# Kernel tuning notes

Hardware: AMD Instinct MI355X
Metric: run time of the kernel (lower is better)

Reference implementation:

```python
import jax, jax.numpy as jnp
import numpy as np

B, S, H, M, STEPS = 8, 1024, 1024, 4, 5
LN_EPS = 1e-5


def _gelu(x):
    return jax.nn.gelu(x, approximate=False)  # torch nn.GELU default is exact erf


def _layernorm(x, g, b):
    mu = jnp.mean(x, axis=-1, keepdims=True)
    var = jnp.mean((x - mu) ** 2, axis=-1, keepdims=True)
    return (x - mu) * jax.lax.rsqrt(var + LN_EPS) * g + b


def setup_inputs() -> dict:
    key = jax.random.key(0)
    ks = jax.random.split(key, 16)
    def w(k, shape, scale=0.02):
        return (jax.random.normal(k, shape) * scale).astype(jnp.float32)
    z = lambda *shape: jnp.zeros(shape, jnp.float32)
    o = lambda *shape: jnp.ones(shape, jnp.float32)
    return {
        "deterministic_state": jax.random.normal(ks[0], (B, S, H), jnp.float32),
        "superposition_state": jax.random.normal(ks[1], (B, S, H * M), jnp.float32),
        "context": jax.random.normal(ks[2], (B, H), jnp.float32),
        # reasoning_mode_selector: Linear(H,H) -> GELU -> Linear(H,2) -> Softmax
        "Wm1": w(ks[3], (H, H)), "bm1": z(H), "Wm2": w(ks[4], (H, 2)), "bm2": z(2),
        # reasoning_depth_controller: Linear(H,H//2) -> GELU -> Linear(H//2,STEPS) -> Softmax
        "Wd1": w(ks[5], (H, H // 2)), "bd1": z(H // 2), "Wd2": w(ks[6], (H // 2, STEPS)), "bd2": z(STEPS),
        # explicit_reasoning_steps (stacked over STEPS): Linear(2H,H)->GELU->Linear(H,H)->LayerNorm
        "We1": w(ks[7], (STEPS, 2 * H, H)), "be1": z(STEPS, H),
        "We2": w(ks[8], (STEPS, H, H)), "be2": z(STEPS, H),
        "ln_g": o(STEPS, H), "ln_b": z(STEPS, H),
        # reasoning_memory GRUCell(H,H); gate order r,z,n as in torch
        "W_ih": w(ks[9], (H, 3 * H)), "W_hh": w(ks[10], (H, 3 * H)),
        "b_ih": z(3 * H), "b_hh": z(3 * H),
        # implicit_reasoning: Linear(H*M,2H)->GELU->Linear(2H,H*M)->LayerNorm
        "Wi1": w(ks[11], (H * M, 2 * H)), "bi1": z(2 * H),
        "Wi2": w(ks[12], (2 * H, H * M)), "bi2": z(H * M),
        "lni_g": o(H * M), "lni_b": z(H * M),
    }


def _forward(deterministic_state, superposition_state, context,
             Wm1, bm1, Wm2, bm2, Wd1, bd1, Wd2, bd2,
             We1, be1, We2, be2, ln_g, ln_b,
             W_ih, W_hh, b_ih, b_hh,
             Wi1, bi1, Wi2, bi2, lni_g, lni_b):
    b, s, h = deterministic_state.shape
    # mode / depth selection from 2D context [B,H]
    mode_weights = jax.nn.softmax(_gelu(context @ Wm1 + bm1) @ Wm2 + bm2, axis=-1)   # [B,2]
    depth_weights = jax.nn.softmax(_gelu(context @ Wd1 + bd1) @ Wd2 + bd2, axis=-1)  # [B,STEPS]

    ctx_exp = jnp.broadcast_to(context[:, None, :], (b, s, h))  # context.unsqueeze(1).expand

    def gru_cell(x, hprev):  # x,hprev: [N,H]
        gi = x @ W_ih + b_ih
        gh = hprev @ W_hh + b_hh
        i_r, i_z, i_n = jnp.split(gi, 3, axis=-1)
        h_r, h_z, h_n = jnp.split(gh, 3, axis=-1)
        r = jax.nn.sigmoid(i_r + h_r)
        z = jax.nn.sigmoid(i_z + h_z)
        n = jnp.tanh(i_n + r * h_n)
        return (1.0 - z) * n + z * hprev

    def step(carry, params):
        state, memory = carry
        W1, b1, W2, b2, g, beta = params
        combined = jnp.concatenate([state, ctx_exp], axis=-1)          # [B,S,2H]
        next_state = _layernorm(_gelu(combined @ W1 + b1) @ W2 + b2, g, beta)
        mem = gru_cell(next_state.reshape(-1, h), memory.reshape(-1, h)).reshape(b, s, h)
        gated = next_state + 0.1 * mem
        return (gated, mem), gated

    init = (deterministic_state, jnp.zeros_like(deterministic_state))
    _, gated_states = jax.lax.scan(step, init, (We1, be1, We2, be2, ln_g, ln_b))  # [STEPS,B,S,H]
    explicit_result = jnp.einsum('bi,ibsh->bsh', depth_weights, gated_states)

    implicit_result = _layernorm(_gelu(superposition_state @ Wi1 + bi1) @ Wi2 + bi2, lni_g, lni_b)  # [B,S,M*H]
    implicit_det = implicit_result.reshape(b, s, M, h).mean(axis=2)  # [B,S,H]

    result = (mode_weights[:, 0, None, None] * implicit_det
              + mode_weights[:, 1, None, None] * explicit_result)
    return result, mode_weights, depth_weights, explicit_result, implicit_result


def reference(deterministic_state, superposition_state, context,
              Wm1, bm1, Wm2, bm2, Wd1, bd1, Wd2, bd2,
              We1, be1, We2, be2, ln_g, ln_b,
              W_ih, W_hh, b_ih, b_hh,
              Wi1, bi1, Wi2, bi2, lni_g, lni_b):
    return _forward(deterministic_state, superposition_state, context,
                    Wm1, bm1, Wm2, bm2, Wd1, bd1, Wd2, bd2,
                    We1, be1, We2, be2, ln_g, ln_b,
                    W_ih, W_hh, b_ih, b_hh,
                    Wi1, bi1, Wi2, bi2, lni_g, lni_b)
```

## Files before the change

### kernel.cpp

```cpp
#include <hip/hip_runtime.h>
#include <hip/hip_bf16.h>
#include <math.h>


typedef unsigned short bf16_t;
typedef __attribute__((ext_vector_type(8))) short s8v;
typedef __attribute__((ext_vector_type(4))) float f4v;

typedef const __attribute__((address_space(1))) void* gas_ptr;
typedef __attribute__((address_space(3))) void* las_ptr;

#define DEVFN static __device__ __forceinline__

DEVFN bf16_t f2b(float f) {
    union { float f; unsigned u; } v; v.f = f;
    unsigned r = v.u + 0x7FFFu + ((v.u >> 16) & 1u);
    return (bf16_t)(r >> 16);
}
DEVFN float b2f(bf16_t b) {
    union { unsigned u; float f; } v; v.u = ((unsigned)b) << 16; return v.f;
}
DEVFN float geluf(float x) { return 0.5f * x * (1.0f + erff(x * 0.70710678118654752f)); }
DEVFN float sigmf(float x) { return 1.0f / (1.0f + expf(-x)); }

template <int N_> DEVFN void waitvm() {
    if constexpr (N_ == 7)  asm volatile("s_waitcnt vmcnt(7)"  ::: "memory");
    if constexpr (N_ == 9)  asm volatile("s_waitcnt vmcnt(9)"  ::: "memory");
    if constexpr (N_ == 10) asm volatile("s_waitcnt vmcnt(10)" ::: "memory");
    if constexpr (N_ == 12) asm volatile("s_waitcnt vmcnt(12)" ::: "memory");
    __builtin_amdgcn_sched_barrier(0);
}
DEVFN void lgkm0() {
    asm volatile("s_waitcnt lgkmcnt(0)" ::: "memory");
    __builtin_amdgcn_sched_barrier(0);
}

static const long OUT_RESULT = 0;
static const long OUT_MODE   = 8388608;
static const long OUT_DEPTH  = 8388624;
static const long OUT_EXPL   = 8388664;
static const long OUT_IMPL   = 16777272;

#define READ_AH(mh, c_) { _Pragma("unroll") \
    for (int mf = 0; mf < MF / 2; ++mf) { _Pragma("unroll") \
      for (int ks = 0; ks < 2; ++ks) { \
        aR[mf][ks] = *(const s8v*)(lds + (c_) * BUFB + \
            ((mh) * (BM / 2) + wm * (BM / 4) + mf * 16 + l15) * 128 + \
            ((((ks << 2) + lhi) ^ l7) << 4)); } } }

#define READ_BH(nh, c_, dst) { _Pragma("unroll") \
    for (int nf = 0; nf < NF / 2; ++nf) { _Pragma("unroll") \
      for (int ks = 0; ks < 2; ++ks) { \
        dst[nf][ks] = *(const s8v*)(lds + (c_) * BUFB + ABYTES + \
            ((nh) * (BN / 2) + wn * (BN / 8) + nf * 16 + l15) * 128 + \
            ((((ks << 2) + lhi) ^ l7) << 4)); } } }

#define MFMA_Q(mh, nh, bset) { __builtin_amdgcn_s_setprio(1); _Pragma("unroll") \
    for (int mf = 0; mf < MF / 2; ++mf) { _Pragma("unroll") \
      for (int nf = 0; nf < NF / 2; ++nf) { _Pragma("unroll") \
        for (int ks = 0; ks < 2; ++ks) { \
          acc[(mh) * (MF / 2) + mf][(nh) * (NF / 2) + nf] = \
            __builtin_amdgcn_mfma_f32_16x16x32_bf16(aR[mf][ks], bset[nf][ks], \
                acc[(mh) * (MF / 2) + mf][(nh) * (NF / 2) + nf], 0, 0, 0); } } } \
    __builtin_amdgcn_s_setprio(0); }

template <int MF, int NF, int EPI>
__global__ __launch_bounds__(512, 2) void gemm8p(
    const bf16_t* __restrict__ A, const bf16_t* __restrict__ Bt,
    const float* __restrict__ bias, bf16_t* __restrict__ outB, int N, int K)
{
    constexpr int BM = MF * 32;
    constexpr int BN = NF * 64;
    constexpr int LA = BM / 64;
    constexpr int LB = BN / 64;
    constexpr int sA = LA / 2;
    constexpr int sB = LB / 2;
    constexpr int V1 = 3 * sA + 2 * sB;
    constexpr int V24 = 3 * (sA + sB);
    constexpr int ABYTES = BM * 128;
    constexpr int BUFB = (BM + BN) * 128;

    __shared__ __align__(16) char lds[2 * BUFB];

    const int tid  = threadIdx.x;
    const int lane = tid & 63;
    const int wave = tid >> 6;
    const int wm = wave >> 2, wn = wave & 3;
    const int l15 = lane & 15, lhi = lane >> 4, l7 = lane & 7;

    const int gx = gridDim.x;
    const int nwg = gx * gridDim.y;
    const int orig = blockIdx.y * gx + blockIdx.x;
    const int qq = nwg >> 3, rr8 = nwg & 7;
    const int xcd = orig & 7, lid = orig >> 3;
    const int nid = (xcd < rr8 ? xcd * (qq + 1) : rr8 * (qq + 1) + (xcd - rr8) * qq) + lid;
    const int m0 = (nid / gx) * BM;
    const int n0 = (nid % gx) * BN;

    const int NT = K >> 6;

    f4v acc[MF][NF];
#pragma unroll
    for (int i = 0; i < MF; ++i)
#pragma unroll
        for (int j = 0; j < NF; ++j)
#pragma unroll
            for (int q2 = 0; q2 < 4; ++q2) acc[i][j][q2] = 0.0f;

    s8v aR[MF / 2][2];
    s8v bR0[NF / 2][2], bR1[NF / 2][2];

    auto stageA = [&](int ts, int tb, int h) {
        const int kt = ts << 6;
#pragma unroll
        for (int i = 0; i < sA; ++i) {
            const int li = (h * sA + i) * 512 + tid;
            const int r = li >> 3, s = li & 7;
            const bf16_t* src = A + (long)(m0 + r) * K + kt + ((s ^ (r & 7)) << 3);
            __builtin_amdgcn_global_load_lds((gas_ptr)src, (las_ptr)(lds + tb * BUFB + li * 16), 16, 0, 0);
        }
    };
    auto stageB = [&](int ts, int tb, int h) {
        const int kt = ts << 6;
#pragma unroll
        for (int i = 0; i < sB; ++i) {
            const int li = (h * sB + i) * 512 + tid;
            const int r = li >> 3, s = li & 7;
            const bf16_t* src = Bt + (long)(n0 + r) * K + kt + ((s ^ (r & 7)) << 3);
            __builtin_amdgcn_global_load_lds((gas_ptr)src, (las_ptr)(lds + tb * BUFB + ABYTES + li * 16), 16, 0, 0);
        }
    };

    stageA(0, 0, 0); stageB(0, 0, 0); stageB(0, 0, 1); stageA(0, 0, 1);
    stageA(1, 1, 0); stageB(1, 1, 0); stageB(1, 1, 1); stageA(1, 1, 1);
    waitvm<V24>();
    __builtin_amdgcn_s_barrier();

    for (int t = 0; t < NT; ++t) {
        const int c = t & 1;
        int ts = t + 2; if (ts >= NT) ts -= NT;
        READ_AH(0, c);
        READ_BH(0, c, bR0);
        waitvm<V1>();
        __builtin_amdgcn_s_barrier();
        lgkm0();
        MFMA_Q(0, 0, bR0);
        __builtin_amdgcn_s_barrier();
        READ_BH(1, c, bR1);
        stageA(ts, c, 0); stageB(ts, c, 0);
        waitvm<V24>();
        __builtin_amdgcn_s_barrier();
        lgkm0();
        MFMA_Q(0, 1, bR1);
        __builtin_amdgcn_s_barrier();
        READ_AH(1, c);
        stageB(ts, c, 1);
        __builtin_amdgcn_s_barrier();
        lgkm0();
        MFMA_Q(1, 1, bR1);
        __builtin_amdgcn_s_barrier();
        stageA(ts, c, 1);
        waitvm<V24>();
        __builtin_amdgcn_s_barrier();
        MFMA_Q(1, 0, bR0);
        __builtin_amdgcn_s_barrier();
    }

    const int crr = lhi << 2;
#pragma unroll
    for (int mh = 0; mh < 2; ++mh) {
#pragma unroll
        for (int mf = 0; mf < MF / 2; ++mf) {
#pragma unroll
            for (int nh = 0; nh < 2; ++nh) {
#pragma unroll
                for (int nf = 0; nf < NF / 2; ++nf) {
                    const int col = n0 + nh * (BN / 2) + wn * (BN / 8) + nf * 16 + l15;
#pragma unroll
                    for (int q2 = 0; q2 < 4; ++q2) {
                        const int row = m0 + mh * (BM / 2) + wm * (BM / 4) + mf * 16 + crr + q2;
                        const float v = acc[mh * (MF / 2) + mf][nh * (NF / 2) + nf][q2];
                        if (EPI == 1) {
                            outB[(long)row * N + col] = f2b(geluf(v + bias[col]));
                        } else if (EPI == 2) {
                            outB[(long)row * N + col] = f2b(geluf(v + bias[(long)(row >> 10) * N + col]));
                        } else {
                            outB[(long)row * N + col] = f2b(v + bias[col]);
                        }
                    }
                }
            }
        }
    }
}

__global__ __launch_bounds__(256) void transpose_k(
    const float* __restrict__ src, bf16_t* __restrict__ dst,
    int K, int N, long sbs, long dbs)
{
    __shared__ float tile[32][33];
    const float* s = src + (long)blockIdx.z * sbs;
    bf16_t* d = dst + (long)blockIdx.z * dbs;
    const int n0 = blockIdx.x * 32, k0 = blockIdx.y * 32;
    const int tx = threadIdx.x, ty = threadIdx.y;
#pragma unroll
    for (int i = 0; i < 4; ++i)
        tile[ty + i * 8][tx] = s[(long)(k0 + ty + i * 8) * N + n0 + tx];
    __syncthreads();
#pragma unroll
    for (int i = 0; i < 4; ++i)
        d[(long)(n0 + ty + i * 8) * K + k0 + tx] = f2b(tile[tx][ty + i * 8]);
}

__global__ __launch_bounds__(256) void cvt_k(const float4* __restrict__ src,
                                             ushort4* __restrict__ dst, int n4)
{
    const int i = blockIdx.x * 256 + threadIdx.x;
    if (i < n4) {
        float4 v = src[i];
        ushort4 o; o.x = f2b(v.x); o.y = f2b(v.y); o.z = f2b(v.z); o.w = f2b(v.w);
        dst[i] = o;
    }
}

__global__ __launch_bounds__(256) void colgemv8_k(
    const float* __restrict__ ctx, const float* __restrict__ Wbase, long wts,
    int Wld, const float* __restrict__ bias, long bts,
    float* __restrict__ out, long ots, int do_gelu)
{
    __shared__ float cs[8][1024];
    __shared__ float rr[16][16][8];
    const int j0 = blockIdx.x * 16;
    const int t = blockIdx.y;
    const int tid = threadIdx.x;
    for (int i = tid; i < 2048; i += 256)
        ((float4*)cs)[i] = ((const float4*)ctx)[i];
    __syncthreads();
    const int kp = tid >> 4, jj = tid & 15;
    const float* Wp = Wbase + (long)t * wts;
    float p[8] = {0, 0, 0, 0, 0, 0, 0, 0};
    for (int i = 0; i < 64; ++i) {
        const int k = kp * 64 + i;
        const float w = Wp[(long)k * Wld + j0 + jj];
#pragma unroll
        for (int b = 0; b < 8; ++b) p[b] = fmaf(cs[b][k], w, p[b]);
    }
#pragma unroll
    for (int b = 0; b < 8; ++b) rr[kp][jj][b] = p[b];
    __syncthreads();
    if (tid < 128) {
        const int jj2 = tid >> 3, b = tid & 7;
        float s = 0.f;
#pragma unroll
        for (int k2 = 0; k2 < 16; ++k2) s += rr[k2][jj2][b];
        s += bias[(long)t * bts + j0 + jj2];
        if (do_gelu) s = geluf(s);
        out[(long)t * ots + (long)b * Wld + j0 + jj2] = s;
    }
}

__global__ __launch_bounds__(256) void selB_k(
    const float* __restrict__ h1, const float* __restrict__ hd,
    const float* __restrict__ Wm2, const float* __restrict__ bm2,
    const float* __restrict__ Wd2, const float* __restrict__ bd2,
    float* __restrict__ outM, float* __restrict__ outD,
    float* __restrict__ wsM, float* __restrict__ wsD)
{
    const int b = blockIdx.x, tid = threadIdx.x;
    __shared__ float red[256];
    float lm[2], ld[5];
    for (int o = 0; o < 2; ++o) {
        float p = 0.f;
        for (int k = tid; k < 1024; k += 256) p += h1[b * 1024 + k] * Wm2[k * 2 + o];
        red[tid] = p; __syncthreads();
        for (int s = 128; s > 0; s >>= 1) { if (tid < s) red[tid] += red[tid + s]; __syncthreads(); }
        lm[o] = red[0] + bm2[o]; __syncthreads();
    }
    for (int o = 0; o < 5; ++o) {
        float p = 0.f;
        for (int k = tid; k < 512; k += 256) p += hd[b * 512 + k] * Wd2[k * 5 + o];
        red[tid] = p; __syncthreads();
        for (int s = 128; s > 0; s >>= 1) { if (tid < s) red[tid] += red[tid + s]; __syncthreads(); }
        ld[o] = red[0] + bd2[o]; __syncthreads();
    }
    if (tid == 0) {
        float mx = fmaxf(lm[0], lm[1]);
        float e0 = expf(lm[0] - mx), e1 = expf(lm[1] - mx);
        float inv = 1.f / (e0 + e1);
        outM[b * 2] = e0 * inv; outM[b * 2 + 1] = e1 * inv;
        wsM[b * 2] = e0 * inv;  wsM[b * 2 + 1] = e1 * inv;
        float md = ld[0];
        for (int o = 1; o < 5; ++o) md = fmaxf(md, ld[o]);
        float es[5]; float sum = 0.f;
        for (int o = 0; o < 5; ++o) { es[o] = expf(ld[o] - md); sum += es[o]; }
        for (int o = 0; o < 5; ++o) { outD[b * 5 + o] = es[o] / sum; wsD[b * 5 + o] = es[o] / sum; }
    }
}

__global__ __launch_bounds__(256) void ln1024_k(
    const bf16_t* __restrict__ X, const float* __restrict__ g,
    const float* __restrict__ b, bf16_t* __restrict__ Yb)
{
    const int row = blockIdx.x, tid = threadIdx.x;
    const ushort4 xv = ((const ushort4*)(X + (long)row * 1024))[tid];
    const float x0 = b2f(xv.x), x1 = b2f(xv.y), x2 = b2f(xv.z), x3 = b2f(xv.w);
    float s = x0 + x1 + x2 + x3;
    float ss = x0 * x0 + x1 * x1 + x2 * x2 + x3 * x3;
#pragma unroll
    for (int o = 32; o > 0; o >>= 1) { s += __shfl_down(s, o); ss += __shfl_down(ss, o); }
    __shared__ float rs[4], rss[4];
    const int wv = tid >> 6, ln = tid & 63;
    if (ln == 0) { rs[wv] = s; rss[wv] = ss; }
    __syncthreads();
    const float S = rs[0] + rs[1] + rs[2] + rs[3];
    const float SS = rss[0] + rss[1] + rss[2] + rss[3];
    const float mean = S * (1.0f / 1024.0f);
    const float var = SS * (1.0f / 1024.0f) - mean * mean;
    const float rstd = rsqrtf(var + 1e-5f);
    const float4 gv = ((const float4*)g)[tid];
    const float4 bv = ((const float4*)b)[tid];
    ushort4 ob;
    ob.x = f2b((x0 - mean) * rstd * gv.x + bv.x);
    ob.y = f2b((x1 - mean) * rstd * gv.y + bv.y);
    ob.z = f2b((x2 - mean) * rstd * gv.z + bv.z);
    ob.w = f2b((x3 - mean) * rstd * gv.w + bv.w);
    ((ushort4*)(Yb + (long)row * 1024))[tid] = ob;
}

template <bool FIRST>
__global__ __launch_bounds__(256) void gru_k(
    const bf16_t* __restrict__ gi, const bf16_t* __restrict__ gh,
    const float* __restrict__ bhh, const bf16_t* __restrict__ nsB,
    bf16_t* __restrict__ memB, bf16_t* __restrict__ stateB,
    float* __restrict__ expl, const float* __restrict__ depthw, int t)
{
    const long i4 = (long)blockIdx.x * 256 + threadIdx.x;
    const long row = i4 >> 8;
    const int h4 = (int)(i4 & 255) << 2;
    const bf16_t* gir = gi + row * 3072 + h4;
    const ushort4 vir = *(const ushort4*)(gir);
    const ushort4 viz = *(const ushort4*)(gir + 1024);
    const ushort4 vin = *(const ushort4*)(gir + 2048);
    float hr[4], hz[4], hn[4];
    if (FIRST) {
        const float4 a = *(const float4*)(bhh + h4);
        const float4 c = *(const float4*)(bhh + 1024 + h4);
        const float4 d = *(const float4*)(bhh + 2048 + h4);
        hr[0] = a.x; hr[1] = a.y; hr[2] = a.z; hr[3] = a.w;
        hz[0] = c.x; hz[1] = c.y; hz[2] = c.z; hz[3] = c.w;
        hn[0] = d.x; hn[1] = d.y; hn[2] = d.z; hn[3] = d.w;
    } else {
        const bf16_t* ghr = gh + row * 3072 + h4;
        const ushort4 g1 = *(const ushort4*)(ghr);
        const ushort4 g2 = *(const ushort4*)(ghr + 1024);
        const ushort4 g3 = *(const ushort4*)(ghr + 2048);
        hr[0] = b2f(g1.x); hr[1] = b2f(g1.y); hr[2] = b2f(g1.z); hr[3] = b2f(g1.w);
        hz[0] = b2f(g2.x); hz[1] = b2f(g2.y); hz[2] = b2f(g2.z); hz[3] = b2f(g2.w);
        hn[0] = b2f(g3.x); hn[1] = b2f(g3.y); hn[2] = b2f(g3.z); hn[3] = b2f(g3.w);
    }
    const ushort4 nsv = *(const ushort4*)(nsB + row * 1024 + h4);
    float mo[4] = {0.f, 0.f, 0.f, 0.f};
    if (!FIRST) {
        const ushort4 mv = *(const ushort4*)(memB + row * 1024 + h4);
        mo[0] = b2f(mv.x); mo[1] = b2f(mv.y); mo[2] = b2f(mv.z); mo[3] = b2f(mv.w);
    }
    const float dw = depthw[(int)(row >> 10) * 5 + t];
    const float ir[4] = {b2f(vir.x), b2f(vir.y), b2f(vir.z), b2f(vir.w)};
    const float iz[4] = {b2f(viz.x), b2f(viz.y), b2f(viz.z), b2f(viz.w)};
    const float in_[4] = {b2f(vin.x), b2f(vin.y), b2f(vin.z), b2f(vin.w)};
    const float ns[4] = {b2f(nsv.x), b2f(nsv.y), b2f(nsv.z), b2f(nsv.w)};
    ushort4 mnb, stb; float4 exv;
    float mn[4], gt[4];
#pragma unroll
    for (int i = 0; i < 4; ++i) {
        const float rg = sigmf(ir[i] + hr[i]);
        const float zg = sigmf(iz[i] + hz[i]);
        const float ng = tanhf(in_[i] + rg * hn[i]);
        mn[i] = (1.0f - zg) * ng + zg * mo[i];
        gt[i] = ns[i] + 0.1f * mn[i];
    }
    mnb.x = f2b(mn[0]); mnb.y = f2b(mn[1]); mnb.z = f2b(mn[2]); mnb.w = f2b(mn[3]);
    stb.x = f2b(gt[0]); stb.y = f2b(gt[1]); stb.z = f2b(gt[2]); stb.w = f2b(gt[3]);
    exv.x = dw * gt[0]; exv.y = dw * gt[1]; exv.z = dw * gt[2]; exv.w = dw * gt[3];
    *(ushort4*)(memB + row * 1024 + h4) = mnb;
    *(ushort4*)(stateB + row * 1024 + h4) = stb;
    float* ep = expl + row * 1024 + h4;
    if (FIRST) {
        *(float4*)ep = exv;
    } else {
        float4 old = *(const float4*)ep;
        old.x += exv.x; old.y += exv.y; old.z += exv.z; old.w += exv.w;
        *(float4*)ep = old;
    }
}

__global__ __launch_bounds__(1024) void ln4096_final_k(
    const bf16_t* __restrict__ Ypre, const float* __restrict__ g,
    const float* __restrict__ b, const float* __restrict__ expl,
    float* __restrict__ implOut, float* __restrict__ result,
    const float* __restrict__ modew)
{
    const int row = blockIdx.x, tid = threadIdx.x;
    const ushort4 xv = ((const ushort4*)(Ypre + (long)row * 4096))[tid];
    const float x0 = b2f(xv.x), x1 = b2f(xv.y), x2 = b2f(xv.z), x3 = b2f(xv.w);
    float s = x0 + x1 + x2 + x3;
    float ss = x0 * x0 + x1 * x1 + x2 * x2 + x3 * x3;
#pragma unroll
    for (int o = 32; o > 0; o >>= 1) { s += __shfl_down(s, o); ss += __shfl_down(ss, o); }
    __shared__ float rs[16], rss[16];
    __shared__ float ylds[4096];
    const int wv = tid >> 6, ln = tid & 63;
    if (ln == 0) { rs[wv] = s; rss[wv] = ss; }
    __syncthreads();
    if (tid < 64) {
        float a = (ln < 16) ? rs[ln] : 0.f;
        float c2 = (ln < 16) ? rss[ln] : 0.f;
#pragma unroll
        for (int o = 8; o > 0; o >>= 1) { a += __shfl_down(a, o); c2 += __shfl_down(c2, o); }
        if (ln == 0) { rs[0] = a; rss[0] = c2; }
    }
    __syncthreads();
    const float mean = rs[0] * (1.f / 4096.f);
    const float var = rss[0] * (1.f / 4096.f) - mean * mean;
    const float rstd = rsqrtf(var + 1e-5f);
    const float4 gv = ((const float4*)g)[tid];
    const float4 bv = ((const float4*)b)[tid];
    float4 y;
    y.x = (x0 - mean) * rstd * gv.x + bv.x;
    y.y = (x1 - mean) * rstd * gv.y + bv.y;
    y.z = (x2 - mean) * rstd * gv.z + bv.z;
    y.w = (x3 - mean) * rstd * gv.w + bv.w;
    ((float4*)(implOut + (long)row * 4096))[tid] = y;
    ((float4*)ylds)[tid] = y;
    __syncthreads();
    const int bidx = row >> 10;
    const float det4 = 0.25f * (ylds[tid] + ylds[tid + 1024] + ylds[tid + 2048] + ylds[tid + 3072]);
    result[(long)row * 1024 + tid] = modew[bidx * 2] * det4
                                   + modew[bidx * 2 + 1] * expl[(long)row * 1024 + tid];
}

extern "C" void kernel_launch(void* const* d_in, const int* in_sizes, int n_in,
                              void* d_out, int out_size, void* d_ws, size_t ws_size,
                              hipStream_t stream)
{
    const float* det    = (const float*)d_in[0];
    const float* super_ = (const float*)d_in[1];
    const float* ctx    = (const float*)d_in[2];
    const float* Wm1 = (const float*)d_in[3];
    const float* bm1 = (const float*)d_in[4];
    const float* Wm2 = (const float*)d_in[5];
    const float* bm2 = (const float*)d_in[6];
    const float* Wd1 = (const float*)d_in[7];
    const float* bd1 = (const float*)d_in[8];
    const float* Wd2 = (const float*)d_in[9];
    const float* bd2 = (const float*)d_in[10];
    const float* We1 = (const float*)d_in[11];
    const float* be1 = (const float*)d_in[12];
    const float* We2 = (const float*)d_in[13];
    const float* be2 = (const float*)d_in[14];
    const float* ln_g = (const float*)d_in[15];
    const float* ln_b = (const float*)d_in[16];
    const float* W_ih = (const float*)d_in[17];
    const float* W_hh = (const float*)d_in[18];
    const float* b_ih = (const float*)d_in[19];
    const float* b_hh = (const float*)d_in[20];
    const float* Wi1 = (const float*)d_in[21];
    const float* bi1 = (const float*)d_in[22];
    const float* Wi2 = (const float*)d_in[23];
    const float* bi2 = (const float*)d_in[24];
    const float* lni_g = (const float*)d_in[25];
    const float* lni_b = (const float*)d_in[26];

    float* out = (float*)d_out;
    char* W = (char*)d_ws;

    bf16_t* We1sT = (bf16_t*)(W + 0);
    bf16_t* We2T  = (bf16_t*)(W + 10485760L);
    bf16_t* WihT  = (bf16_t*)(W + 20971520L);
    bf16_t* WhhT  = (bf16_t*)(W + 27262976L);
    bf16_t* Wi1T  = (bf16_t*)(W + 33554432L);
    bf16_t* Wi2T  = (bf16_t*)(W + 50331648L);
    float* ctxbias = (float*)(W + 67108864L);
    float* modew   = (float*)(W + 67272704L);
    float* depthw  = (float*)(W + 67272768L);
    float* h1ws    = (float*)(W + 67276800L);
    float* hdws    = (float*)(W + 67309568L);
    const long SB = 67325952L;
    bf16_t* stateb = (bf16_t*)(W + SB);
    bf16_t* Zb     = (bf16_t*)(W + SB + 16777216L);
    bf16_t* memb   = (bf16_t*)(W + SB + 50331648L);
    bf16_t* nsB    = (bf16_t*)(W + SB + 67108864L);
    bf16_t* gi     = (bf16_t*)(W + SB + 83886080L);
    bf16_t* gh     = (bf16_t*)(W + SB + 134217728L);
    bf16_t* Y1     = gi;
    bf16_t* superb = gi;
    bf16_t* Yi     = (bf16_t*)(W + SB + 83886080L + 67108864L);
    bf16_t* Ypre   = gi;

    (void)in_sizes; (void)n_in; (void)out_size; (void)ws_size;

    dim3 tb(32, 8);

    colgemv8_k<<<dim3(64, 1), 256, 0, stream>>>(ctx, Wm1, 0, 1024, bm1, 0, h1ws, 0, 1);
    colgemv8_k<<<dim3(32, 1), 256, 0, stream>>>(ctx, Wd1, 0, 512, bd1, 0, hdws, 0, 1);
    colgemv8_k<<<dim3(64, 5), 256, 0, stream>>>(ctx, We1 + 1048576L, 2097152L, 1024,
                                                be1, 1024, ctxbias, 8192, 0);
    selB_k<<<8, 256, 0, stream>>>(h1ws, hdws, Wm2, bm2, Wd2, bd2,
                                  out + OUT_MODE, out + OUT_DEPTH, modew, depthw);

    transpose_k<<<dim3(32, 32, 5), tb, 0, stream>>>(We1, We1sT, 1024, 1024, 2097152L, 1048576L);
    transpose_k<<<dim3(32, 32, 5), tb, 0, stream>>>(We2, We2T, 1024, 1024, 1048576L, 1048576L);
    transpose_k<<<dim3(96, 32, 1), tb, 0, stream>>>(W_ih, WihT, 1024, 3072, 0L, 0L);
    transpose_k<<<dim3(96, 32, 1), tb, 0, stream>>>(W_hh, WhhT, 1024, 3072, 0L, 0L);
    transpose_k<<<dim3(64, 128, 1), tb, 0, stream>>>(Wi1, Wi1T, 4096, 2048, 0L, 0L);
    transpose_k<<<dim3(128, 64, 1), tb, 0, stream>>>(Wi2, Wi2T, 2048, 4096, 0L, 0L);

    cvt_k<<<8192, 256, 0, stream>>>((const float4*)det, (ushort4*)stateb, 2097152);

    for (int t = 0; t < 5; ++t) {
        gemm8p<4, 4, 2><<<dim3(4, 64), 512, 0, stream>>>(stateb, We1sT + (long)t * 1048576,
                                                         ctxbias + (long)t * 8192, Y1, 1024, 1024);
        gemm8p<4, 4, 3><<<dim3(4, 64), 512, 0, stream>>>(Y1, We2T + (long)t * 1048576,
                                                         be2 + t * 1024, Zb, 1024, 1024);
        ln1024_k<<<8192, 256, 0, stream>>>(Zb, ln_g + t * 1024, ln_b + t * 1024, nsB);
        gemm8p<4, 4, 3><<<dim3(12, 64), 512, 0, stream>>>(nsB, WihT, b_ih, gi, 3072, 1024);
        if (t > 0)
            gemm8p<4, 4, 3><<<dim3(12, 64), 512, 0, stream>>>(memb, WhhT, b_hh, gh, 3072, 1024);
        if (t == 0)
            gru_k<true><<<8192, 256, 0, stream>>>(gi, gh, b_hh, nsB, memb, stateb,
                                                  out + OUT_EXPL, depthw, t);
        else
            gru_k<false><<<8192, 256, 0, stream>>>(gi, gh, b_hh, nsB, memb, stateb,
                                                   out + OUT_EXPL, depthw, t);
    }

    cvt_k<<<32768, 256, 0, stream>>>((const float4*)super_, (ushort4*)superb, 8388608);
    gemm8p<8, 4, 1><<<dim3(8, 32), 512, 0, stream>>>(superb, Wi1T, bi1, Yi, 2048, 4096);
    gemm8p<8, 4, 3><<<dim3(16, 32), 512, 0, stream>>>(Yi, Wi2T, bi2, Ypre, 4096, 2048);
    ln4096_final_k<<<8192, 1024, 0, stream>>>(Ypre, lni_g, lni_b, out + OUT_EXPL,
                                              out + OUT_IMPL, out + OUT_RESULT, modew);
}
```

Measured before the change: 1.482 ms.

## Precompute GEMM address pointers, unroll K loop by two, defer explicit accumulation to final kernel

The GEMM main loop now keeps per-thread global source pointers that are advanced each K tile. LDS read offsets, including the swizzle, are hoisted out of the loop. The loop is unrolled by two with a peeled tail that issues no wasted wraparound loads. The GRU kernel no longer does the fp32 read-modify-write of the explicit result each step; instead every step's bf16 state is kept in a slab and the final layernorm kernel computes the depth-weighted sum. This removes five fp32 read/write passes over the output but adds five bf16 reads and a larger workspace.

After: 1.477 ms. No clear change (-0.3%).

```diff
diff --git a/kernel.cpp b/kernel.cpp
--- a/kernel.cpp
+++ b/kernel.cpp
@@ -41,19 +41,17 @@
 static const long OUT_EXPL   = 8388664;
 static const long OUT_IMPL   = 16777272;
 
-#define READ_AH(mh, c_) { _Pragma("unroll") \
-    for (int mf = 0; mf < MF / 2; ++mf) { _Pragma("unroll") \
-      for (int ks = 0; ks < 2; ++ks) { \
-        aR[mf][ks] = *(const s8v*)(lds + (c_) * BUFB + \
-            ((mh) * (BM / 2) + wm * (BM / 4) + mf * 16 + l15) * 128 + \
-            ((((ks << 2) + lhi) ^ l7) << 4)); } } }
-
-#define READ_BH(nh, c_, dst) { _Pragma("unroll") \
-    for (int nf = 0; nf < NF / 2; ++nf) { _Pragma("unroll") \
-      for (int ks = 0; ks < 2; ++ks) { \
-        dst[nf][ks] = *(const s8v*)(lds + (c_) * BUFB + ABYTES + \
-            ((nh) * (BN / 2) + wn * (BN / 8) + nf * 16 + l15) * 128 + \
-            ((((ks << 2) + lhi) ^ l7) << 4)); } } }
+static const long SLAB = 8388608;
+
+#define RD_A(mh, c_) { _Pragma("unroll") \
+    for (int mf = 0; mf < MF / 2; ++mf) { \
+        aR[mf][0] = *(const s8v*)(lds + (c_) * BUFB + aL + kof0 + ((mh) * (BM / 2) + mf * 16) * 128); \
+        aR[mf][1] = *(const s8v*)(lds + (c_) * BUFB + aL + kof1 + ((mh) * (BM / 2) + mf * 16) * 128); } }
+
+#define RD_B(nh, c_, dst) { _Pragma("unroll") \
+    for (int nf = 0; nf < NF / 2; ++nf) { \
+        dst[nf][0] = *(const s8v*)(lds + (c_) * BUFB + bL + kof0 + ((nh) * (BN / 2) + nf * 16) * 128); \
+        dst[nf][1] = *(const s8v*)(lds + (c_) * BUFB + bL + kof1 + ((nh) * (BN / 2) + nf * 16) * 128); } }
 
 #define MFMA_Q(mh, nh, bset) { __builtin_amdgcn_s_setprio(1); _Pragma("unroll") \
     for (int mf = 0; mf < MF / 2; ++mf) { _Pragma("unroll") \
@@ -63,6 +61,33 @@
             __builtin_amdgcn_mfma_f32_16x16x32_bf16(aR[mf][ks], bset[nf][ks], \
                 acc[(mh) * (MF / 2) + mf][(nh) * (NF / 2) + nf], 0, 0, 0); } } } \
     __builtin_amdgcn_s_setprio(0); }
+
+#define KTILE(c_, STG) {                                            \
+    RD_A(0, c_); RD_B(0, c_, bR0);                                  \
+    waitvm<V1>();                                                   \
+    __builtin_amdgcn_s_barrier();                                   \
+    lgkm0();                                                        \
+    MFMA_Q(0, 0, bR0);                                              \
+    __builtin_amdgcn_s_barrier();                                   \
+    RD_B(1, c_, bR1);                                               \
+    if (STG) { stgA(0, c_); stgB(0, c_); }                          \
+    waitvm<V24>();                                                  \
+    __builtin_amdgcn_s_barrier();                                   \
+    lgkm0();                                                        \
+    MFMA_Q(0, 1, bR1);                                              \
+    __builtin_amdgcn_s_barrier();                                   \
+    RD_A(1, c_);                                                    \
+    if (STG) { stgB(1, c_); }                                       \
+    __builtin_amdgcn_s_barrier();                                   \
+    lgkm0();                                                        \
+    MFMA_Q(1, 1, bR1);                                              \
+    __builtin_amdgcn_s_barrier();                                   \
+    if (STG) { stgA(1, c_); }                                       \
+    waitvm<V24>();                                                  \
+    __builtin_amdgcn_s_barrier();                                   \
+    MFMA_Q(1, 0, bR0);                                              \
+    __builtin_amdgcn_s_barrier();                                   \
+}
 
 template <int MF, int NF, int EPI>
 __global__ __launch_bounds__(512, 2) void gemm8p(
@@ -99,6 +124,13 @@
 
     const int NT = K >> 6;
 
+    const int b2k = l7 >> 2;
+    const int lx  = lhi ^ (l7 & 3);
+    const unsigned aL   = (unsigned)((wm * (BM / 4) + l15) * 128 + (lx << 4));
+    const unsigned bL   = (unsigned)(ABYTES + (wn * (BN / 8) + l15) * 128 + (lx << 4));
+    const unsigned kof0 = (unsigned)(b2k << 6);
+    const unsigned kof1 = (unsigned)((b2k ^ 1) << 6);
+
     f4v acc[MF][NF];
 #pragma unroll
     for (int i = 0; i < MF; ++i)
@@ -110,61 +142,54 @@
     s8v aR[MF / 2][2];
     s8v bR0[NF / 2][2], bR1[NF / 2][2];
 
-    auto stageA = [&](int ts, int tb, int h) {
-        const int kt = ts << 6;
-#pragma unroll
-        for (int i = 0; i < sA; ++i) {
-            const int li = (h * sA + i) * 512 + tid;
-            const int r = li >> 3, s = li & 7;
-            const bf16_t* src = A + (long)(m0 + r) * K + kt + ((s ^ (r & 7)) << 3);
-            __builtin_amdgcn_global_load_lds((gas_ptr)src, (las_ptr)(lds + tb * BUFB + li * 16), 16, 0, 0);
-        }
+    const bf16_t* pA[LA];
+    const bf16_t* pB[LB];
+#pragma unroll
+    for (int i = 0; i < LA; ++i) {
+        const int li = i * 512 + tid;
+        const int r = li >> 3, s = li & 7;
+        pA[i] = A + (long)(m0 + r) * K + ((s ^ (r & 7)) << 3);
+    }
+#pragma unroll
+    for (int i = 0; i < LB; ++i) {
+        const int li = i * 512 + tid;
+        const int r = li >> 3, s = li & 7;
+        pB[i] = Bt + (long)(n0 + r) * K + ((s ^ (r & 7)) << 3);
+    }
+
+    auto stgA = [&](int h, int cbuf) {
+#pragma unroll
+        for (int i = 0; i < sA; ++i)
+            __builtin_amdgcn_global_load_lds((gas_ptr)pA[h * sA + i],
+                (las_ptr)(lds + cbuf * BUFB + (h * sA + i) * 8192 + tid * 16), 16, 0, 0);
     };
-    auto stageB = [&](int ts, int tb, int h) {
-        const int kt = ts << 6;
-#pragma unroll
-        for (int i = 0; i < sB; ++i) {
-            const int li = (h * sB + i) * 512 + tid;
-            const int r = li >> 3, s = li & 7;
-            const bf16_t* src = Bt + (long)(n0 + r) * K + kt + ((s ^ (r & 7)) << 3);
-            __builtin_amdgcn_global_load_lds((gas_ptr)src, (las_ptr)(lds + tb * BUFB + ABYTES + li * 16), 16, 0, 0);
-        }
+    auto stgB = [&](int h, int cbuf) {
+#pragma unroll
+        for (int i = 0; i < sB; ++i)
+            __builtin_amdgcn_global_load_lds((gas_ptr)pB[h * sB + i],
+                (las_ptr)(lds + cbuf * BUFB + ABYTES + (h * sB + i) * 8192 + tid * 16), 16, 0, 0);
     };
-
-    stageA(0, 0, 0); stageB(0, 0, 0); stageB(0, 0, 1); stageA(0, 0, 1);
-    stageA(1, 1, 0); stageB(1, 1, 0); stageB(1, 1, 1); stageA(1, 1, 1);
+    auto adv = [&]() {
+#pragma unroll
+        for (int i = 0; i < LA; ++i) pA[i] += 64;
+#pragma unroll
+        for (int i = 0; i < LB; ++i) pB[i] += 64;
+    };
+
+    stgA(0, 0); stgB(0, 0); stgB(1, 0); stgA(1, 0); adv();
+    stgA(0, 1); stgB(0, 1); stgB(1, 1); stgA(1, 1); adv();
     waitvm<V24>();
     __builtin_amdgcn_s_barrier();
 
-    for (int t = 0; t < NT; ++t) {
-        const int c = t & 1;
-        int ts = t + 2; if (ts >= NT) ts -= NT;
-        READ_AH(0, c);
-        READ_BH(0, c, bR0);
-        waitvm<V1>();
-        __builtin_amdgcn_s_barrier();
-        lgkm0();
-        MFMA_Q(0, 0, bR0);
-        __builtin_amdgcn_s_barrier();
-        READ_BH(1, c, bR1);
-        stageA(ts, c, 0); stageB(ts, c, 0);
-        waitvm<V24>();
-        __builtin_amdgcn_s_barrier();
-        lgkm0();
-        MFMA_Q(0, 1, bR1);
-        __builtin_amdgcn_s_barrier();
-        READ_AH(1, c);
-        stageB(ts, c, 1);
-        __builtin_amdgcn_s_barrier();
-        lgkm0();
-        MFMA_Q(1, 1, bR1);
-        __builtin_amdgcn_s_barrier();
-        stageA(ts, c, 1);
-        waitvm<V24>();
-        __builtin_amdgcn_s_barrier();
-        MFMA_Q(1, 0, bR0);
-        __builtin_amdgcn_s_barrier();
-    }
+    for (int t = 0; t < NT - 2; t += 2) {
+        KTILE(0, true);  adv();
+        KTILE(1, true);  adv();
+    }
+    asm volatile("s_waitcnt vmcnt(0)" ::: "memory");
+    __builtin_amdgcn_sched_barrier(0);
+    __builtin_amdgcn_s_barrier();
+    KTILE(0, false);
+    KTILE(1, false);
 
     const int crr = lhi << 2;
 #pragma unroll
@@ -331,8 +356,7 @@
 __global__ __launch_bounds__(256) void gru_k(
     const bf16_t* __restrict__ gi, const bf16_t* __restrict__ gh,
     const float* __restrict__ bhh, const bf16_t* __restrict__ nsB,
-    bf16_t* __restrict__ memB, bf16_t* __restrict__ stateB,
-    float* __restrict__ expl, const float* __restrict__ depthw, int t)
+    bf16_t* __restrict__ memB, bf16_t* __restrict__ stateOut)
 {
     const long i4 = (long)blockIdx.x * 256 + threadIdx.x;
     const long row = i4 >> 8;
@@ -364,12 +388,11 @@
         const ushort4 mv = *(const ushort4*)(memB + row * 1024 + h4);
         mo[0] = b2f(mv.x); mo[1] = b2f(mv.y); mo[2] = b2f(mv.z); mo[3] = b2f(mv.w);
     }
-    const float dw = depthw[(int)(row >> 10) * 5 + t];
     const float ir[4] = {b2f(vir.x), b2f(vir.y), b2f(vir.z), b2f(vir.w)};
     const float iz[4] = {b2f(viz.x), b2f(viz.y), b2f(viz.z), b2f(viz.w)};
     const float in_[4] = {b2f(vin.x), b2f(vin.y), b2f(vin.z), b2f(vin.w)};
     const float ns[4] = {b2f(nsv.x), b2f(nsv.y), b2f(nsv.z), b2f(nsv.w)};
-    ushort4 mnb, stb; float4 exv;
+    ushort4 mnb, stb;
     float mn[4], gt[4];
 #pragma unroll
     for (int i = 0; i < 4; ++i) {
@@ -381,23 +404,15 @@
     }
     mnb.x = f2b(mn[0]); mnb.y = f2b(mn[1]); mnb.z = f2b(mn[2]); mnb.w = f2b(mn[3]);
     stb.x = f2b(gt[0]); stb.y = f2b(gt[1]); stb.z = f2b(gt[2]); stb.w = f2b(gt[3]);
-    exv.x = dw * gt[0]; exv.y = dw * gt[1]; exv.z = dw * gt[2]; exv.w = dw * gt[3];
     *(ushort4*)(memB + row * 1024 + h4) = mnb;
-    *(ushort4*)(stateB + row * 1024 + h4) = stb;
-    float* ep = expl + row * 1024 + h4;
-    if (FIRST) {
-        *(float4*)ep = exv;
-    } else {
-        float4 old = *(const float4*)ep;
-        old.x += exv.x; old.y += exv.y; old.z += exv.z; old.w += exv.w;
-        *(float4*)ep = old;
-    }
+    *(ushort4*)(stateOut + row * 1024 + h4) = stb;
 }
 
 __global__ __launch_bounds__(1024) void ln4096_final_k(
     const bf16_t* __restrict__ Ypre, const float* __restrict__ g,
-    const float* __restrict__ b, const float* __restrict__ expl,
-    float* __restrict__ implOut, float* __restrict__ result,
+    const float* __restrict__ b, const bf16_t* __restrict__ stS,
+    const float* __restrict__ depthw, float* __restrict__ implOut,
+    float* __restrict__ explOut, float* __restrict__ result,
     const float* __restrict__ modew)
 {
     const int row = blockIdx.x, tid = threadIdx.x;
@@ -434,9 +449,14 @@
     ((float4*)ylds)[tid] = y;
     __syncthreads();
     const int bidx = row >> 10;
+    const long off = (long)row * 1024 + tid;
+    float ex = 0.f;
+#pragma unroll
+    for (int tt = 0; tt < 5; ++tt)
+        ex += depthw[bidx * 5 + tt] * b2f(stS[(long)tt * SLAB + off]);
+    explOut[off] = ex;
     const float det4 = 0.25f * (ylds[tid] + ylds[tid + 1024] + ylds[tid + 2048] + ylds[tid + 3072]);
-    result[(long)row * 1024 + tid] = modew[bidx * 2] * det4
-                                   + modew[bidx * 2 + 1] * expl[(long)row * 1024 + tid];
+    result[off] = modew[bidx * 2] * det4 + modew[bidx * 2 + 1] * ex;
 }
 
 extern "C" void kernel_launch(void* const* d_in, const int* in_sizes, int n_in,
@@ -486,15 +506,15 @@
     float* h1ws    = (float*)(W + 67276800L);
     float* hdws    = (float*)(W + 67309568L);
     const long SB = 67325952L;
-    bf16_t* stateb = (bf16_t*)(W + SB);
-    bf16_t* Zb     = (bf16_t*)(W + SB + 16777216L);
-    bf16_t* memb   = (bf16_t*)(W + SB + 50331648L);
-    bf16_t* nsB    = (bf16_t*)(W + SB + 67108864L);
-    bf16_t* gi     = (bf16_t*)(W + SB + 83886080L);
-    bf16_t* gh     = (bf16_t*)(W + SB + 134217728L);
+    bf16_t* stateS = (bf16_t*)(W + SB);
+    bf16_t* Zb     = (bf16_t*)(W + SB + 100663296L);
+    bf16_t* memb   = (bf16_t*)(W + SB + 117440512L);
+    bf16_t* nsB    = (bf16_t*)(W + SB + 134217728L);
+    bf16_t* gi     = (bf16_t*)(W + SB + 150994944L);
+    bf16_t* gh     = (bf16_t*)(W + SB + 201326592L);
     bf16_t* Y1     = gi;
     bf16_t* superb = gi;
-    bf16_t* Yi     = (bf16_t*)(W + SB + 83886080L + 67108864L);
+    bf16_t* Yi     = (bf16_t*)(W + SB + 201326592L + 16777216L);
     bf16_t* Ypre   = gi;
 
     (void)in_sizes; (void)n_in; (void)out_size; (void)ws_size;
@@ -515,10 +535,12 @@
     transpose_k<<<dim3(64, 128, 1), tb, 0, stream>>>(Wi1, Wi1T, 4096, 2048, 0L, 0L);
     transpose_k<<<dim3(128, 64, 1), tb, 0, stream>>>(Wi2, Wi2T, 2048, 4096, 0L, 0L);
 
-    cvt_k<<<8192, 256, 0, stream>>>((const float4*)det, (ushort4*)stateb, 2097152);
+    cvt_k<<<8192, 256, 0, stream>>>((const float4*)det, (ushort4*)stateS, 2097152);
 
     for (int t = 0; t < 5; ++t) {
-        gemm8p<4, 4, 2><<<dim3(4, 64), 512, 0, stream>>>(stateb, We1sT + (long)t * 1048576,
+        const bf16_t* stIn = stateS + (long)t * SLAB;
+        bf16_t* stOut = stateS + (long)(t + 1) * SLAB;
+        gemm8p<4, 4, 2><<<dim3(4, 64), 512, 0, stream>>>(stIn, We1sT + (long)t * 1048576,
                                                          ctxbias + (long)t * 8192, Y1, 1024, 1024);
         gemm8p<4, 4, 3><<<dim3(4, 64), 512, 0, stream>>>(Y1, We2T + (long)t * 1048576,
                                                          be2 + t * 1024, Zb, 1024, 1024);
@@ -527,16 +549,15 @@
         if (t > 0)
             gemm8p<4, 4, 3><<<dim3(12, 64), 512, 0, stream>>>(memb, WhhT, b_hh, gh, 3072, 1024);
         if (t == 0)
-            gru_k<true><<<8192, 256, 0, stream>>>(gi, gh, b_hh, nsB, memb, stateb,
-                                                  out + OUT_EXPL, depthw, t);
+            gru_k<true><<<8192, 256, 0, stream>>>(gi, gh, b_hh, nsB, memb, stOut);
         else
-            gru_k<false><<<8192, 256, 0, stream>>>(gi, gh, b_hh, nsB, memb, stateb,
-                                                   out + OUT_EXPL, depthw, t);
+            gru_k<false><<<8192, 256, 0, stream>>>(gi, gh, b_hh, nsB, memb, stOut);
     }
 
     cvt_k<<<32768, 256, 0, stream>>>((const float4*)super_, (ushort4*)superb, 8388608);
     gemm8p<8, 4, 1><<<dim3(8, 32), 512, 0, stream>>>(superb, Wi1T, bi1, Yi, 2048, 4096);
     gemm8p<8, 4, 3><<<dim3(16, 32), 512, 0, stream>>>(Yi, Wi2T, bi2, Ypre, 4096, 2048);
-    ln4096_final_k<<<8192, 1024, 0, stream>>>(Ypre, lni_g, lni_b, out + OUT_EXPL,
-                                              out + OUT_IMPL, out + OUT_RESULT, modew);
-}
+    ln4096_final_k<<<8192, 1024, 0, stream>>>(Ypre, lni_g, lni_b, stateS + SLAB, depthw,
+                                              out + OUT_IMPL, out + OUT_EXPL,
+                                              out + OUT_RESULT, modew);
+}
```
